# Performance work log

Hardware: AMD Instinct MI355X
Metric: run time of the kernel (lower is better)

Reference implementation:

```python
import jax, jax.numpy as jnp
import numpy as np

B, L, D, S = 32, 1024, 1024, 32
TAU = 1.0


def setup_inputs() -> dict:
    key = jax.random.key(0)
    ks = jax.random.split(key, 13)
    s = 0.02
    return {
        "x": jax.random.normal(ks[0], (B, L, D), dtype=jnp.float32),
        # state_encoder: Linear(D,D) -> ReLU -> Linear(D,S)
        "enc_w1": jax.random.normal(ks[1], (D, D), dtype=jnp.float32) * s,
        "enc_b1": jnp.zeros((D,), dtype=jnp.float32),
        "enc_w2": jax.random.normal(ks[2], (D, S), dtype=jnp.float32) * s,
        "enc_b2": jnp.zeros((S,), dtype=jnp.float32),
        # transition_learner: Linear(S,2S) -> ReLU -> Linear(2S,S*S)
        "tr_w1": jax.random.normal(ks[3], (S, 2 * S), dtype=jnp.float32) * s,
        "tr_b1": jnp.zeros((2 * S,), dtype=jnp.float32),
        "tr_w2": jax.random.normal(ks[4], (2 * S, S * S), dtype=jnp.float32) * s,
        "tr_b2": jnp.zeros((S * S,), dtype=jnp.float32),
        # state_decoder: Linear(S,D) -> ReLU -> Linear(D,D)
        "dec_w1": jax.random.normal(ks[5], (S, D), dtype=jnp.float32) * s,
        "dec_b1": jnp.zeros((D,), dtype=jnp.float32),
        "dec_w2": jax.random.normal(ks[6], (D, D), dtype=jnp.float32) * s,
        "dec_b2": jnp.zeros((D,), dtype=jnp.float32),
    }


def reference(x, enc_w1, enc_b1, enc_w2, enc_b2,
              tr_w1, tr_b1, tr_w2, tr_b2,
              dec_w1, dec_b1, dec_w2, dec_b2):
    b, l, d = x.shape
    # state encoder + softmax over states  -> [B, L, S]
    h = jax.nn.relu(x @ enc_w1 + enc_b1)
    state_probs = jax.nn.softmax((h @ enc_w2 + enc_b2) / TAU, axis=-1)
    # transition matrices: batch all L-1 timesteps in one GEMM pass
    cur = state_probs[:, :-1, :]                      # [B, L-1, S]
    th = jax.nn.relu(cur @ tr_w1 + tr_b1)             # [B, L-1, 2S]
    tl = th @ tr_w2 + tr_b2                           # [B, L-1, S*S]
    s = state_probs.shape[-1]
    trans = jax.nn.softmax(tl.reshape(b, l - 1, s, s) / TAU, axis=-1)
    # state decoder  -> [B, L, D]
    dh = jax.nn.relu(state_probs @ dec_w1 + dec_b1)
    markov_out = dh @ dec_w2 + dec_b2
    return markov_out, trans
```

## Files before the change

kernel.cpp:

```cpp
#include <hip/hip_runtime.h>
#include <hip/hip_bf16.h>
#include <cstdint>
#include <cstddef>

typedef __attribute__((ext_vector_type(4))) float  f32x4;
typedef __attribute__((ext_vector_type(8))) __bf16 bf16x8;
typedef __attribute__((ext_vector_type(4))) __bf16 bf16x4;

#define DEV __device__ __forceinline__

DEV void gload_lds16(const void* g, void* l) {
  __builtin_amdgcn_global_load_lds(
      (const __attribute__((address_space(1))) void*)g,
      (__attribute__((address_space(3))) void*)l, 16, 0, 0);
}

DEV float wave16_max(float v) {
#pragma unroll
  for (int s = 1; s < 16; s <<= 1) v = fmaxf(v, __shfl_xor(v, s, 64));
  return v;
}
DEV float wave16_sum(float v) {
#pragma unroll
  for (int s = 1; s < 16; s <<= 1) v += __shfl_xor(v, s, 64);
  return v;
}

__global__ __launch_bounds__(256) void cvt_f32_bf16(
    const float* __restrict__ in, __bf16* __restrict__ out, int n4) {
  int i = blockIdx.x * 256 + threadIdx.x;
  if (i < n4) {
    f32x4 v = ((const f32x4*)in)[i];
    ((bf16x4*)out)[i] = __builtin_convertvector(v, bf16x4);
  }
}

__global__ void transpose_cvt(const float* __restrict__ in,
                              __bf16* __restrict__ out, int R, int C) {
  __shared__ float tile[32][33];
  int c0 = blockIdx.x * 32, r0 = blockIdx.y * 32;
  int tx = threadIdx.x, ty = threadIdx.y;
#pragma unroll
  for (int i = ty; i < 32; i += 8)
    tile[i][tx] = in[(size_t)(r0 + i) * C + c0 + tx];
  __syncthreads();
#pragma unroll
  for (int i = ty; i < 32; i += 8)
    out[(size_t)(c0 + i) * R + r0 + tx] = (__bf16)tile[tx][i];
}

template <int RELU, int OUT_BF16>
__global__ __launch_bounds__(256) void gemm128(
    const __bf16* __restrict__ A, const __bf16* __restrict__ BT,
    const float* __restrict__ bias, void* __restrict__ Cout,
    int M, int N, int K) {
  __shared__ __bf16 As[128 * 64];
  __shared__ __bf16 Bs[128 * 64];
  const int nbc = N >> 7;
  const int bid = blockIdx.x;
  const int br = bid / nbc, bc = bid - br * nbc;
  const int t = threadIdx.x;
  const int w = t >> 6, l = t & 63;
  const int wr = w >> 1, wc = w & 1;
  const int lr = l & 15, lg = l >> 4;

  f32x4 acc[4][4];
  const f32x4 z = {0.f, 0.f, 0.f, 0.f};
#pragma unroll
  for (int m = 0; m < 4; ++m)
#pragma unroll
    for (int n = 0; n < 4; ++n) acc[m][n] = z;

  const __bf16* gA = A + (size_t)(br * 128 + (t >> 3)) * K + (t & 7) * 8;
  const __bf16* gB = BT + (size_t)(bc * 128 + (t >> 3)) * K + (t & 7) * 8;
  char* lA = (char*)As + t * 16;
  char* lB = (char*)Bs + t * 16;

  for (int kt = 0; kt < K; kt += 64) {
    __syncthreads();
#pragma unroll
    for (int r = 0; r < 4; ++r) {
      gload_lds16(gA + (size_t)r * 32 * K + kt, lA + r * 4096);
      gload_lds16(gB + (size_t)r * 32 * K + kt, lB + r * 4096);
    }
    __syncthreads();
#pragma unroll
    for (int kk = 0; kk < 2; ++kk) {
      bf16x8 af[4], bf[4];
#pragma unroll
      for (int m = 0; m < 4; ++m)
        af[m] = *(const bf16x8*)(As + (wr * 64 + m * 16 + lr) * 64 + kk * 32 + lg * 8);
#pragma unroll
      for (int n = 0; n < 4; ++n)
        bf[n] = *(const bf16x8*)(Bs + (wc * 64 + n * 16 + lr) * 64 + kk * 32 + lg * 8);
#pragma unroll
      for (int m = 0; m < 4; ++m)
#pragma unroll
        for (int n = 0; n < 4; ++n)
          acc[m][n] = __builtin_amdgcn_mfma_f32_16x16x32_bf16(af[m], bf[n], acc[m][n], 0, 0, 0);
    }
  }

#pragma unroll
  for (int n = 0; n < 4; ++n) {
    int col = bc * 128 + wc * 64 + n * 16 + lr;
    float bv = bias[col];
#pragma unroll
    for (int m = 0; m < 4; ++m) {
      int row0 = br * 128 + wr * 64 + m * 16 + lg * 4;
#pragma unroll
      for (int j = 0; j < 4; ++j) {
        float v = acc[m][n][j] + bv;
        if (RELU) v = v > 0.f ? v : 0.f;
        size_t off = (size_t)(row0 + j) * N + col;
        if (OUT_BF16) ((__bf16*)Cout)[off] = (__bf16)v;
        else          ((float*)Cout)[off] = v;
      }
    }
  }
}

__global__ __launch_bounds__(256) void enc2_softmax(
    const __bf16* __restrict__ H, const __bf16* __restrict__ W2T,
    const float* __restrict__ b2, __bf16* __restrict__ P, int K) {
  __shared__ __bf16 As[128 * 64];
  __shared__ __bf16 Bs[32 * 64];
  const int br = blockIdx.x;
  const int t = threadIdx.x;
  const int w = t >> 6, l = t & 63;
  const int lr = l & 15, lg = l >> 4;

  f32x4 acc[2][2];
  const f32x4 z = {0.f, 0.f, 0.f, 0.f};
#pragma unroll
  for (int m = 0; m < 2; ++m)
#pragma unroll
    for (int n = 0; n < 2; ++n) acc[m][n] = z;

  const __bf16* gA = H + (size_t)(br * 128 + (t >> 3)) * K + (t & 7) * 8;
  const __bf16* gB = W2T + (size_t)(t >> 3) * K + (t & 7) * 8;
  char* lA = (char*)As + t * 16;
  char* lB = (char*)Bs + t * 16;

  for (int kt = 0; kt < K; kt += 64) {
    __syncthreads();
#pragma unroll
    for (int r = 0; r < 4; ++r) gload_lds16(gA + (size_t)r * 32 * K + kt, lA + r * 4096);
    gload_lds16(gB + kt, lB);
    __syncthreads();
#pragma unroll
    for (int kk = 0; kk < 2; ++kk) {
      bf16x8 af[2], bf[2];
#pragma unroll
      for (int m = 0; m < 2; ++m)
        af[m] = *(const bf16x8*)(As + (w * 32 + m * 16 + lr) * 64 + kk * 32 + lg * 8);
#pragma unroll
      for (int n = 0; n < 2; ++n)
        bf[n] = *(const bf16x8*)(Bs + (n * 16 + lr) * 64 + kk * 32 + lg * 8);
#pragma unroll
      for (int m = 0; m < 2; ++m)
#pragma unroll
        for (int n = 0; n < 2; ++n)
          acc[m][n] = __builtin_amdgcn_mfma_f32_16x16x32_bf16(af[m], bf[n], acc[m][n], 0, 0, 0);
    }
  }

  float b2lo = b2[lr], b2hi = b2[16 + lr];
#pragma unroll
  for (int m = 0; m < 2; ++m) {
#pragma unroll
    for (int j = 0; j < 4; ++j) {
      float c0 = acc[m][0][j] + b2lo;
      float c1 = acc[m][1][j] + b2hi;
      float mx = wave16_max(fmaxf(c0, c1));
      float e0 = __expf(c0 - mx), e1 = __expf(c1 - mx);
      float sm = wave16_sum(e0 + e1);
      float inv = 1.f / sm;
      int row = br * 128 + w * 32 + m * 16 + lg * 4 + j;
      P[(size_t)row * 32 + lr]      = (__bf16)(e0 * inv);
      P[(size_t)row * 32 + 16 + lr] = (__bf16)(e1 * inv);
    }
  }
}

__global__ __launch_bounds__(256) void trans1(
    const __bf16* __restrict__ P, const __bf16* __restrict__ W1T,
    const float* __restrict__ b1, __bf16* __restrict__ TH, int Mout) {
  const int t = threadIdx.x;
  const int w = t >> 6, l = t & 63;
  const int lr = l & 15, lg = l >> 4;
  const int rowbase = blockIdx.x * 128 + w * 32;

  f32x4 acc[2][4];
  const f32x4 z = {0.f, 0.f, 0.f, 0.f};
#pragma unroll
  for (int m = 0; m < 2; ++m)
#pragma unroll
    for (int n = 0; n < 4; ++n) acc[m][n] = z;

  bf16x8 af[2], bf[4];
#pragma unroll
  for (int m = 0; m < 2; ++m) {
    int orow = rowbase + m * 16 + lr;
    if (orow > Mout - 1) orow = Mout - 1;
    int q = orow / 1023;
    int prow = q * 1024 + (orow - q * 1023);
    af[m] = *(const bf16x8*)(P + (size_t)prow * 32 + lg * 8);
  }
#pragma unroll
  for (int n = 0; n < 4; ++n)
    bf[n] = *(const bf16x8*)(W1T + (n * 16 + lr) * 32 + lg * 8);
#pragma unroll
  for (int m = 0; m < 2; ++m)
#pragma unroll
    for (int n = 0; n < 4; ++n)
      acc[m][n] = __builtin_amdgcn_mfma_f32_16x16x32_bf16(af[m], bf[n], acc[m][n], 0, 0, 0);

#pragma unroll
  for (int n = 0; n < 4; ++n) {
    int col = n * 16 + lr;
    float bv = b1[col];
#pragma unroll
    for (int m = 0; m < 2; ++m) {
      int row0 = rowbase + m * 16 + lg * 4;
#pragma unroll
      for (int j = 0; j < 4; ++j) {
        int row = row0 + j;
        if (row < Mout) {
          float v = acc[m][n][j] + bv;
          v = v > 0.f ? v : 0.f;
          TH[(size_t)row * 64 + col] = (__bf16)v;
        }
      }
    }
  }
}

__global__ __launch_bounds__(256) void trans2_softmax(
    const __bf16* __restrict__ TH, const __bf16* __restrict__ W2T,
    const float* __restrict__ b2, float* __restrict__ out1, int Mout) {
  const int bid = blockIdx.x;
  const int br = bid >> 3, bc = bid & 7;
  const int t = threadIdx.x;
  const int w = t >> 6, l = t & 63;
  const int wr = w >> 1, wc = w & 1;
  const int lr = l & 15, lg = l >> 4;

  f32x4 acc[4][4];
  const f32x4 z = {0.f, 0.f, 0.f, 0.f};
#pragma unroll
  for (int m = 0; m < 4; ++m)
#pragma unroll
    for (int n = 0; n < 4; ++n) acc[m][n] = z;

#pragma unroll
  for (int ks = 0; ks < 2; ++ks) {
    bf16x8 af[4], bf[4];
#pragma unroll
    for (int m = 0; m < 4; ++m) {
      int ar = br * 128 + wr * 64 + m * 16 + lr;
      if (ar > Mout - 1) ar = Mout - 1;
      af[m] = *(const bf16x8*)(TH + (size_t)ar * 64 + ks * 32 + lg * 8);
    }
#pragma unroll
    for (int n = 0; n < 4; ++n) {
      int bn = bc * 128 + wc * 64 + n * 16 + lr;
      bf[n] = *(const bf16x8*)(W2T + (size_t)bn * 64 + ks * 32 + lg * 8);
    }
#pragma unroll
    for (int m = 0; m < 4; ++m)
#pragma unroll
      for (int n = 0; n < 4; ++n)
        acc[m][n] = __builtin_amdgcn_mfma_f32_16x16x32_bf16(af[m], bf[n], acc[m][n], 0, 0, 0);
  }

#pragma unroll
  for (int m = 0; m < 4; ++m) {
    int row0 = br * 128 + wr * 64 + m * 16 + lg * 4;
#pragma unroll
    for (int j = 0; j < 4; ++j) {
      int r = row0 + j;
      bool valid = r < Mout;
#pragma unroll
      for (int g = 0; g < 2; ++g) {
        int c0 = bc * 128 + wc * 64 + g * 32 + lr;
        int c1 = c0 + 16;
        float v0 = acc[m][2 * g][j] + b2[c0];
        float v1 = acc[m][2 * g + 1][j] + b2[c1];
        float mx = wave16_max(fmaxf(v0, v1));
        float e0 = __expf(v0 - mx), e1 = __expf(v1 - mx);
        float sm = wave16_sum(e0 + e1);
        float inv = 1.f / sm;
        if (valid) {
          out1[(size_t)r * 1024 + c0] = e0 * inv;
          out1[(size_t)r * 1024 + c1] = e1 * inv;
        }
      }
    }
  }
}

__global__ __launch_bounds__(256) void dec1(
    const __bf16* __restrict__ P, const __bf16* __restrict__ W1T,
    const float* __restrict__ b1, __bf16* __restrict__ DH) {
  const int bid = blockIdx.x;
  const int br = bid >> 3, bc = bid & 7;
  const int t = threadIdx.x;
  const int w = t >> 6, l = t & 63;
  const int wr = w >> 1, wc = w & 1;
  const int lr = l & 15, lg = l >> 4;

  f32x4 acc[4][4];
  const f32x4 z = {0.f, 0.f, 0.f, 0.f};
#pragma unroll
  for (int m = 0; m < 4; ++m)
#pragma unroll
    for (int n = 0; n < 4; ++n) acc[m][n] = z;

  bf16x8 af[4], bf[4];
#pragma unroll
  for (int m = 0; m < 4; ++m)
    af[m] = *(const bf16x8*)(P + (size_t)(br * 128 + wr * 64 + m * 16 + lr) * 32 + lg * 8);
#pragma unroll
  for (int n = 0; n < 4; ++n)
    bf[n] = *(const bf16x8*)(W1T + (size_t)(bc * 128 + wc * 64 + n * 16 + lr) * 32 + lg * 8);
#pragma unroll
  for (int m = 0; m < 4; ++m)
#pragma unroll
    for (int n = 0; n < 4; ++n)
      acc[m][n] = __builtin_amdgcn_mfma_f32_16x16x32_bf16(af[m], bf[n], acc[m][n], 0, 0, 0);

#pragma unroll
  for (int n = 0; n < 4; ++n) {
    int col = bc * 128 + wc * 64 + n * 16 + lr;
    float bv = b1[col];
#pragma unroll
    for (int m = 0; m < 4; ++m) {
      int row0 = br * 128 + wr * 64 + m * 16 + lg * 4;
#pragma unroll
      for (int j = 0; j < 4; ++j) {
        float v = acc[m][n][j] + bv;
        v = v > 0.f ? v : 0.f;
        DH[(size_t)(row0 + j) * 1024 + col] = (__bf16)v;
      }
    }
  }
}

extern "C" void kernel_launch(void* const* d_in, const int* in_sizes, int n_in,
                              void* d_out, int out_size, void* d_ws, size_t ws_size,
                              hipStream_t stream) {
  const float* x      = (const float*)d_in[0];
  const float* enc_w1 = (const float*)d_in[1];
  const float* enc_b1 = (const float*)d_in[2];
  const float* enc_w2 = (const float*)d_in[3];
  const float* enc_b2 = (const float*)d_in[4];
  const float* tr_w1  = (const float*)d_in[5];
  const float* tr_b1  = (const float*)d_in[6];
  const float* tr_w2  = (const float*)d_in[7];
  const float* tr_b2  = (const float*)d_in[8];
  const float* dec_w1 = (const float*)d_in[9];
  const float* dec_b1 = (const float*)d_in[10];
  const float* dec_w2 = (const float*)d_in[11];
  const float* dec_b2 = (const float*)d_in[12];

  char* ws = (char*)d_ws;
  __bf16* Xbf  = (__bf16*)(ws);
  __bf16* P    = (__bf16*)(ws + 67108864);
  __bf16* TH   = (__bf16*)(ws + 69206016);
  __bf16* w1T  = (__bf16*)(ws + 73400320);
  __bf16* w2T  = (__bf16*)(ws + 75497472);
  __bf16* tw1T = (__bf16*)(ws + 75563008);
  __bf16* tw2T = (__bf16*)(ws + 75567104);
  __bf16* dw1T = (__bf16*)(ws + 75698176);
  __bf16* dw2T = (__bf16*)(ws + 75763712);
  __bf16* DH   = Xbf;

  float* out0 = (float*)d_out;
  float* out1 = out0 + 33554432;
  __bf16* Hbf = (__bf16*)out1;

  cvt_f32_bf16<<<32768, 256, 0, stream>>>(x, Xbf, 8388608);
  transpose_cvt<<<dim3(32, 32), dim3(32, 8), 0, stream>>>(enc_w1, w1T, 1024, 1024);
  transpose_cvt<<<dim3(1, 32),  dim3(32, 8), 0, stream>>>(enc_w2, w2T, 1024, 32);
  transpose_cvt<<<dim3(2, 1),   dim3(32, 8), 0, stream>>>(tr_w1,  tw1T, 32, 64);
  transpose_cvt<<<dim3(32, 2),  dim3(32, 8), 0, stream>>>(tr_w2,  tw2T, 64, 1024);
  transpose_cvt<<<dim3(32, 1),  dim3(32, 8), 0, stream>>>(dec_w1, dw1T, 32, 1024);
  transpose_cvt<<<dim3(32, 32), dim3(32, 8), 0, stream>>>(dec_w2, dw2T, 1024, 1024);

  gemm128<1, 1><<<2048, 256, 0, stream>>>(Xbf, w1T, enc_b1, Hbf, 32768, 1024, 1024);
  enc2_softmax<<<256, 256, 0, stream>>>(Hbf, w2T, enc_b2, P, 1024);
  trans1<<<256, 256, 0, stream>>>(P, tw1T, tr_b1, TH, 32736);
  trans2_softmax<<<2048, 256, 0, stream>>>(TH, tw2T, tr_b2, out1, 32736);
  dec1<<<2048, 256, 0, stream>>>(P, dw1T, dec_b1, DH);
  gemm128<0, 0><<<2048, 256, 0, stream>>>(DH, dw2T, dec_b2, out0, 32768, 1024, 1024);
}
```

Measured before the change: 671.4 us.

## Replace 128x128 GEMM with double-buffered 256x256 pipelined MFMA kernel

Replaces the 128x128-tile GEMM with a 256x256-tile, 512-thread kernel. It double-buffers A and B in a 128 KB LDS area, XOR-swizzles LDS addresses to avoid bank conflicts, remaps block IDs across 8 groups for L2 locality, and interleaves global->LDS loads with MFMA phases using explicit waitcnt, barriers and setprio. The aim is to hide load latency and raise arithmetic intensity for the two 32768x1024x1024 GEMMs. The cost is heavy register pressure (32 accumulator tiles) and the risk of hand-tuned synchronisation errors. The grid shrinks to 512 blocks, so there may be tail effects.

```diff
diff --git a/kernel.cpp b/kernel.cpp
--- a/kernel.cpp
+++ b/kernel.cpp
@@ -25,6 +25,10 @@
   for (int s = 1; s < 16; s <<= 1) v += __shfl_xor(v, s, 64);
   return v;
 }
+
+#define SBAR()  do { __builtin_amdgcn_sched_barrier(0); __builtin_amdgcn_s_barrier(); __builtin_amdgcn_sched_barrier(0); } while (0)
+#define LGKM0() do { asm volatile("s_waitcnt lgkmcnt(0)" ::: "memory"); __builtin_amdgcn_sched_barrier(0); } while (0)
+#define VMW(n)  do { asm volatile("s_waitcnt vmcnt(" #n ")" ::: "memory"); __builtin_amdgcn_sched_barrier(0); } while (0)
 
 __global__ __launch_bounds__(256) void cvt_f32_bf16(
     const float* __restrict__ in, __bf16* __restrict__ out, int n4) {
@@ -50,74 +54,223 @@
 }
 
 template <int RELU, int OUT_BF16>
-__global__ __launch_bounds__(256) void gemm128(
+__global__ __launch_bounds__(512, 2) void gemm256(
     const __bf16* __restrict__ A, const __bf16* __restrict__ BT,
     const float* __restrict__ bias, void* __restrict__ Cout,
     int M, int N, int K) {
-  __shared__ __bf16 As[128 * 64];
-  __shared__ __bf16 Bs[128 * 64];
-  const int nbc = N >> 7;
-  const int bid = blockIdx.x;
+  __shared__ char lds[131072];
+
+  const int nbc = N >> 8;
+  int bid = blockIdx.x;
+  const int cpx = gridDim.x >> 3;
+  bid = (bid & 7) * cpx + (bid >> 3);
   const int br = bid / nbc, bc = bid - br * nbc;
+
   const int t = threadIdx.x;
   const int w = t >> 6, l = t & 63;
-  const int wr = w >> 1, wc = w & 1;
+  const int wr = w >> 2, wc = w & 3;
   const int lr = l & 15, lg = l >> 4;
 
-  f32x4 acc[4][4];
+  const int q0 = w * 2048 + l * 16;
+  const int r0 = q0 >> 7;
+  const int lc = (q0 & 127) ^ ((r0 & 7) << 4);
+
+  const char* gAb = (const char*)A  + ((size_t)(br * 256 + r0) * K) * 2 + lc;
+  const char* gBb = (const char*)BT + ((size_t)(bc * 256 + r0) * K) * 2 + lc;
+  const size_t rowK8   = (size_t)8   * K * 2;
+  const size_t rowK128 = (size_t)128 * K * 2;
+  char* ldsp = (char*)lds;
+  const int ntm = (K >> 6) - 1;
+
+  f32x4 acc[8][4];
   const f32x4 z = {0.f, 0.f, 0.f, 0.f};
 #pragma unroll
-  for (int m = 0; m < 4; ++m)
+  for (int m = 0; m < 8; ++m)
 #pragma unroll
     for (int n = 0; n < 4; ++n) acc[m][n] = z;
 
-  const __bf16* gA = A + (size_t)(br * 128 + (t >> 3)) * K + (t & 7) * 8;
-  const __bf16* gB = BT + (size_t)(bc * 128 + (t >> 3)) * K + (t & 7) * 8;
-  char* lA = (char*)As + t * 16;
-  char* lB = (char*)Bs + t * 16;
-
-  for (int kt = 0; kt < K; kt += 64) {
-    __syncthreads();
-#pragma unroll
-    for (int r = 0; r < 4; ++r) {
-      gload_lds16(gA + (size_t)r * 32 * K + kt, lA + r * 4096);
-      gload_lds16(gB + (size_t)r * 32 * K + kt, lB + r * 4096);
-    }
-    __syncthreads();
-#pragma unroll
-    for (int kk = 0; kk < 2; ++kk) {
-      bf16x8 af[4], bf[4];
-#pragma unroll
-      for (int m = 0; m < 4; ++m)
-        af[m] = *(const bf16x8*)(As + (wr * 64 + m * 16 + lr) * 64 + kk * 32 + lg * 8);
-#pragma unroll
-      for (int n = 0; n < 4; ++n)
-        bf[n] = *(const bf16x8*)(Bs + (wc * 64 + n * 16 + lr) * 64 + kk * 32 + lg * 8);
-#pragma unroll
-      for (int m = 0; m < 4; ++m)
-#pragma unroll
-        for (int n = 0; n < 4; ++n)
-          acc[m][n] = __builtin_amdgcn_mfma_f32_16x16x32_bf16(af[m], bf[n], acc[m][n], 0, 0, 0);
-    }
-  }
+  bf16x8 af[4][2], bf0[2][2], bf1[2][2];
+
+#define STAGE_A(tile, h, b)                                                  \
+  do {                                                                       \
+    const char* _s = gAb + (size_t)(((tile) & ntm) << 7) + ((h) ? rowK128 : 0); \
+    char* _d = ldsp + (b) * 32768 + (h) * 16384 + q0;                        \
+    gload_lds16(_s, _d);                                                     \
+    gload_lds16(_s + rowK8, _d + 1024);                                      \
+  } while (0)
+#define STAGE_B(tile, h, b)                                                  \
+  do {                                                                       \
+    const char* _s = gBb + (size_t)(((tile) & ntm) << 7) + ((h) ? rowK128 : 0); \
+    char* _d = ldsp + 65536 + (b) * 32768 + (h) * 16384 + q0;                \
+    gload_lds16(_s, _d);                                                     \
+    gload_lds16(_s + rowK8, _d + 1024);                                      \
+  } while (0)
+
+#define RD_A(b, m, kk)                                                        \
+  (*(const bf16x8*)(ldsp + (b) * 32768 +                                      \
+                    (wr * 128 + (m) * 16 + lr) * 128 +                        \
+                    (((kk) * 64 + lg * 16) ^ (((wr * 128 + (m) * 16 + lr) & 7) << 4))))
+#define RD_B(b, n, kk)                                                        \
+  (*(const bf16x8*)(ldsp + 65536 + (b) * 32768 +                              \
+                    (wc * 64 + (n) * 16 + lr) * 128 +                         \
+                    (((kk) * 64 + lg * 16) ^ (((wc * 64 + (n) * 16 + lr) & 7) << 4))))
+
+  STAGE_B(0, 0, 0); STAGE_B(0, 1, 0);
+  STAGE_A(0, 0, 0); STAGE_A(0, 1, 0);
+  STAGE_B(1, 0, 1); STAGE_B(1, 1, 1);
+  VMW(4);
+  SBAR();
+
+  const int NI = K >> 7;
+  for (int i = 0; i < NI; ++i) {
+    const int T0 = 2 * i;
+
+#pragma unroll
+    for (int m = 0; m < 4; ++m) { af[m][0] = RD_A(0, m, 0); af[m][1] = RD_A(0, m, 1); }
+#pragma unroll
+    for (int n = 0; n < 2; ++n) { bf0[n][0] = RD_B(0, n, 0); bf0[n][1] = RD_B(0, n, 1); }
+    STAGE_A(T0 + 1, 0, 1);
+    SBAR(); LGKM0();
+    __builtin_amdgcn_s_setprio(1);
+#pragma unroll
+    for (int m = 0; m < 4; ++m)
+#pragma unroll
+      for (int n = 0; n < 2; ++n)
+#pragma unroll
+        for (int kk = 0; kk < 2; ++kk)
+          acc[m][n] = __builtin_amdgcn_mfma_f32_16x16x32_bf16(af[m][kk], bf0[n][kk], acc[m][n], 0, 0, 0);
+    __builtin_amdgcn_s_setprio(0);
+    SBAR();
+
+#pragma unroll
+    for (int n = 0; n < 2; ++n) { bf1[n][0] = RD_B(0, 2 + n, 0); bf1[n][1] = RD_B(0, 2 + n, 1); }
+    STAGE_A(T0 + 1, 1, 1);
+    SBAR(); LGKM0();
+    __builtin_amdgcn_s_setprio(1);
+#pragma unroll
+    for (int m = 0; m < 4; ++m)
+#pragma unroll
+      for (int n = 0; n < 2; ++n)
+#pragma unroll
+        for (int kk = 0; kk < 2; ++kk)
+          acc[m][2 + n] = __builtin_amdgcn_mfma_f32_16x16x32_bf16(af[m][kk], bf1[n][kk], acc[m][2 + n], 0, 0, 0);
+    __builtin_amdgcn_s_setprio(0);
+    SBAR();
+
+#pragma unroll
+    for (int m = 0; m < 4; ++m) { af[m][0] = RD_A(0, 4 + m, 0); af[m][1] = RD_A(0, 4 + m, 1); }
+    STAGE_B(T0 + 2, 0, 0);
+    SBAR(); LGKM0();
+    __builtin_amdgcn_s_setprio(1);
+#pragma unroll
+    for (int m = 0; m < 4; ++m)
+#pragma unroll
+      for (int n = 0; n < 2; ++n)
+#pragma unroll
+        for (int kk = 0; kk < 2; ++kk)
+          acc[4 + m][2 + n] = __builtin_amdgcn_mfma_f32_16x16x32_bf16(af[m][kk], bf1[n][kk], acc[4 + m][2 + n], 0, 0, 0);
+    __builtin_amdgcn_s_setprio(0);
+    SBAR();
+
+    STAGE_B(T0 + 2, 1, 0);
+    VMW(4);
+    SBAR();
+    __builtin_amdgcn_s_setprio(1);
+#pragma unroll
+    for (int m = 0; m < 4; ++m)
+#pragma unroll
+      for (int n = 0; n < 2; ++n)
+#pragma unroll
+        for (int kk = 0; kk < 2; ++kk)
+          acc[4 + m][n] = __builtin_amdgcn_mfma_f32_16x16x32_bf16(af[m][kk], bf0[n][kk], acc[4 + m][n], 0, 0, 0);
+    __builtin_amdgcn_s_setprio(0);
+    SBAR();
+
+#pragma unroll
+    for (int m = 0; m < 4; ++m) { af[m][0] = RD_A(1, m, 0); af[m][1] = RD_A(1, m, 1); }
+#pragma unroll
+    for (int n = 0; n < 2; ++n) { bf0[n][0] = RD_B(1, n, 0); bf0[n][1] = RD_B(1, n, 1); }
+    STAGE_A(T0 + 2, 0, 0);
+    SBAR(); LGKM0();
+    __builtin_amdgcn_s_setprio(1);
+#pragma unroll
+    for (int m = 0; m < 4; ++m)
+#pragma unroll
+      for (int n = 0; n < 2; ++n)
+#pragma unroll
+        for (int kk = 0; kk < 2; ++kk)
+          acc[m][n] = __builtin_amdgcn_mfma_f32_16x16x32_bf16(af[m][kk], bf0[n][kk], acc[m][n], 0, 0, 0);
+    __builtin_amdgcn_s_setprio(0);
+    SBAR();
+
+#pragma unroll
+    for (int n = 0; n < 2; ++n) { bf1[n][0] = RD_B(1, 2 + n, 0); bf1[n][1] = RD_B(1, 2 + n, 1); }
+    STAGE_A(T0 + 2, 1, 0);
+    SBAR(); LGKM0();
+    __builtin_amdgcn_s_setprio(1);
+#pragma unroll
+    for (int m = 0; m < 4; ++m)
+#pragma unroll
+      for (int n = 0; n < 2; ++n)
+#pragma unroll
+        for (int kk = 0; kk < 2; ++kk)
+          acc[m][2 + n] = __builtin_amdgcn_mfma_f32_16x16x32_bf16(af[m][kk], bf1[n][kk], acc[m][2 + n], 0, 0, 0);
+    __builtin_amdgcn_s_setprio(0);
+    SBAR();
+
+#pragma unroll
+    for (int m = 0; m < 4; ++m) { af[m][0] = RD_A(1, 4 + m, 0); af[m][1] = RD_A(1, 4 + m, 1); }
+    STAGE_B(T0 + 3, 0, 1);
+    SBAR(); LGKM0();
+    __builtin_amdgcn_s_setprio(1);
+#pragma unroll
+    for (int m = 0; m < 4; ++m)
+#pragma unroll
+      for (int n = 0; n < 2; ++n)
+#pragma unroll
+        for (int kk = 0; kk < 2; ++kk)
+          acc[4 + m][2 + n] = __builtin_amdgcn_mfma_f32_16x16x32_bf16(af[m][kk], bf1[n][kk], acc[4 + m][2 + n], 0, 0, 0);
+    __builtin_amdgcn_s_setprio(0);
+    SBAR();
+
+    STAGE_B(T0 + 3, 1, 1);
+    VMW(4);
+    SBAR();
+    __builtin_amdgcn_s_setprio(1);
+#pragma unroll
+    for (int m = 0; m < 4; ++m)
+#pragma unroll
+      for (int n = 0; n < 2; ++n)
+#pragma unroll
+        for (int kk = 0; kk < 2; ++kk)
+          acc[4 + m][n] = __builtin_amdgcn_mfma_f32_16x16x32_bf16(af[m][kk], bf0[n][kk], acc[4 + m][n], 0, 0, 0);
+    __builtin_amdgcn_s_setprio(0);
+    SBAR();
+  }
+
+  asm volatile("s_waitcnt vmcnt(0)" ::: "memory");
 
 #pragma unroll
   for (int n = 0; n < 4; ++n) {
-    int col = bc * 128 + wc * 64 + n * 16 + lr;
-    float bv = bias[col];
-#pragma unroll
-    for (int m = 0; m < 4; ++m) {
-      int row0 = br * 128 + wr * 64 + m * 16 + lg * 4;
+    const int col = bc * 256 + wc * 64 + n * 16 + lr;
+    const float bv = bias[col];
+#pragma unroll
+    for (int m = 0; m < 8; ++m) {
+      const int row0 = br * 256 + wr * 128 + m * 16 + lg * 4;
 #pragma unroll
       for (int j = 0; j < 4; ++j) {
         float v = acc[m][n][j] + bv;
         if (RELU) v = v > 0.f ? v : 0.f;
-        size_t off = (size_t)(row0 + j) * N + col;
+        const size_t off = (size_t)(row0 + j) * N + col;
         if (OUT_BF16) ((__bf16*)Cout)[off] = (__bf16)v;
         else          ((float*)Cout)[off] = v;
       }
     }
   }
+#undef STAGE_A
+#undef STAGE_B
+#undef RD_A
+#undef RD_B
 }
 
 __global__ __launch_bounds__(256) void enc2_softmax(
@@ -388,10 +541,10 @@
   transpose_cvt<<<dim3(32, 1),  dim3(32, 8), 0, stream>>>(dec_w1, dw1T, 32, 1024);
   transpose_cvt<<<dim3(32, 32), dim3(32, 8), 0, stream>>>(dec_w2, dw2T, 1024, 1024);
 
-  gemm128<1, 1><<<2048, 256, 0, stream>>>(Xbf, w1T, enc_b1, Hbf, 32768, 1024, 1024);
+  gemm256<1, 1><<<512, 512, 0, stream>>>(Xbf, w1T, enc_b1, Hbf, 32768, 1024, 1024);
   enc2_softmax<<<256, 256, 0, stream>>>(Hbf, w2T, enc_b2, P, 1024);
   trans1<<<256, 256, 0, stream>>>(P, tw1T, tr_b1, TH, 32736);
   trans2_softmax<<<2048, 256, 0, stream>>>(TH, tw2T, tr_b2, out1, 32736);
   dec1<<<2048, 256, 0, stream>>>(P, dw1T, dec_b1, DH);
-  gemm128<0, 0><<<2048, 256, 0, stream>>>(DH, dw2T, dec_b2, out0, 32768, 1024, 1024);
-}
+  gemm256<0, 0><<<512, 512, 0, stream>>>(DH, dw2T, dec_b2, out0, 32768, 1024, 1024);
+}
```

Result: faster. 619.6 us (-7.7%).
